# Optimization experiments

Hardware: AMD Instinct MI355X
Metric: run time of the kernel (lower is better)

Reference implementation:

```python
import jax, jax.numpy as jnp
import numpy as np

NL, B, L1, L2, D = 4, 64, 256, 256, 1024
LOGIT_SCALE = 1.0
BN_EPS = 1e-8


def setup_inputs() -> dict:
    key = jax.random.key(0)
    k1, k2, k3, k4, k5, k6 = jax.random.split(key, 6)
    reps1 = jax.random.normal(k1, (NL, B, L1, D), dtype=jnp.float32)
    reps2 = jax.random.normal(k2, (NL, B, L2, D), dtype=jnp.float32)
    len1 = jax.random.randint(k3, (B,), 1, L1 + 1)
    len2 = jax.random.randint(k4, (B,), 1, L2 + 1)
    w = jax.random.normal(k5, (1, NL), dtype=jnp.float32) * 0.1
    b = jax.random.normal(k6, (1,), dtype=jnp.float32) * 0.1
    return {"reps1": reps1, "reps2": reps2, "len1": len1, "len2": len2, "w": w, "b": b}


def reference(reps1, reps2, len1, len2, w, b):
    # reps: (NL, B, L, D) hidden states of selected layers, already (B-major per layer)
    neg = jnp.finfo(reps1.dtype).min
    # cosine-normalize along feature dim
    h1 = reps1 / jnp.linalg.norm(reps1, axis=-1, keepdims=True)
    h2 = reps2 / jnp.linalg.norm(reps2, axis=-1, keepdims=True)
    # similarity matrices for all layers at once: (NL, B, L1, L2)
    dots = jnp.einsum("lbid,lbjd->lbij", h1, h2)
    # ragged validity masks
    mask1 = jnp.arange(L1)[None, :] < len1[:, None]  # (B, L1)
    mask2 = jnp.arange(L2)[None, :] < len2[:, None]  # (B, L2)
    n1 = len1.astype(dots.dtype)
    n2 = len2.astype(dots.dtype)
    # max over valid rows i, mean over valid cols j  -> s1 (NL, B)
    max_i = jnp.max(jnp.where(mask1[None, :, :, None], dots, neg), axis=2)  # (NL,B,L2)
    s1 = jnp.sum(jnp.where(mask2[None], max_i, 0.0), axis=2) / n2[None]
    # max over valid cols j, mean over valid rows i  -> s2 (NL, B)
    max_j = jnp.max(jnp.where(mask2[None, :, None, :], dots, neg), axis=3)  # (NL,B,L1)
    s2 = jnp.sum(jnp.where(mask1[None], max_j, 0.0), axis=2) / n1[None]
    # harmonic mean (F1)
    feat = (2.0 * s1 * s2 / (s1 + s2)).T  # (B, NL)
    # BatchNorm1d(affine=False), training mode: batch stats, biased variance
    mean = jnp.mean(feat, axis=0, keepdims=True)
    var = jnp.mean((feat - mean) ** 2, axis=0, keepdims=True)
    feat = (feat - mean) / jnp.sqrt(var + BN_EPS)
    # final linear head + logit scale -> (B,)
    return LOGIT_SCALE * (feat @ w.T + b)[:, 0]
```

## Files before the change

kernel.cpp:

```cpp
#include <hip/hip_runtime.h>

#define NLAYERS 4
#define BATCH   64
#define LEN1    256
#define LEN2    256
#define DIM     1024
#define BKK     32
#define NKT     (DIM / BKK)
#define PITCH   40

typedef _Float16 f16x8 __attribute__((ext_vector_type(8)));
typedef float    f32x4 __attribute__((ext_vector_type(4)));

__global__ __launch_bounds__(1024, 4)
void bs_main(const float* __restrict__ reps1, const float* __restrict__ reps2,
             const int* __restrict__ len1, const int* __restrict__ len2,
             float* __restrict__ feat) {
  __shared__ _Float16 Ah[2][LEN1 * PITCH];
  __shared__ _Float16 Bh[2][LEN2 * PITCH];
  __shared__ float ssq1[LEN1];
  __shared__ float ssq2[LEN2];
  __shared__ float rowp[LEN1][4];
  __shared__ float colp[LEN2][4];
  __shared__ float redbuf[32];

  const int bid = blockIdx.x;
  const int nl  = bid >> 6;
  const int bb  = bid & 63;
  const float* gA = reps1 + (size_t)bid * LEN1 * DIM;
  const float* gB = reps2 + (size_t)bid * LEN2 * DIM;

  const int tid  = threadIdx.x;
  const int lane = tid & 63;
  const int wid  = tid >> 6;
  const int wm   = wid >> 2;
  const int wn   = wid & 3;
  const int li   = lane & 15;
  const int lh   = lane >> 4;

  if (tid < 256)                  ssq1[tid] = 0.0f;
  else if (tid < 512)             ssq2[tid - 256] = 0.0f;

  f32x4 acc[4][4];
  #pragma unroll
  for (int a = 0; a < 4; ++a)
    #pragma unroll
    for (int c = 0; c < 4; ++c) acc[a][c] = 0.0f;

  float pssqA = 0.f, pssqB = 0.f;
  const int rS = tid >> 2;
  const int cS = (tid & 3) * 8;

  float4 ra[2], rb[2];

  auto issue_loads = [&](int kt) {
    const float4* a4 = (const float4*)(gA + (size_t)rS * DIM + kt * BKK + cS);
    ra[0] = a4[0];  ra[1] = a4[1];
    const float4* b4 = (const float4*)(gB + (size_t)rS * DIM + kt * BKK + cS);
    rb[0] = b4[0];  rb[1] = b4[1];
  };

  auto convert_write = [&](int buf) {
    const int idx = rS * PITCH + cS;
    {
      const float f0 = ra[0].x, f1 = ra[0].y, f2 = ra[0].z, f3 = ra[0].w;
      const float f4 = ra[1].x, f5 = ra[1].y, f6 = ra[1].z, f7 = ra[1].w;
      pssqA += f0*f0 + f1*f1 + f2*f2 + f3*f3 + f4*f4 + f5*f5 + f6*f6 + f7*f7;
      f16x8 hv;
      hv[0] = (_Float16)f0; hv[1] = (_Float16)f1; hv[2] = (_Float16)f2; hv[3] = (_Float16)f3;
      hv[4] = (_Float16)f4; hv[5] = (_Float16)f5; hv[6] = (_Float16)f6; hv[7] = (_Float16)f7;
      *(f16x8*)&Ah[buf][idx] = hv;
    }
    {
      const float f0 = rb[0].x, f1 = rb[0].y, f2 = rb[0].z, f3 = rb[0].w;
      const float f4 = rb[1].x, f5 = rb[1].y, f6 = rb[1].z, f7 = rb[1].w;
      pssqB += f0*f0 + f1*f1 + f2*f2 + f3*f3 + f4*f4 + f5*f5 + f6*f6 + f7*f7;
      f16x8 hv;
      hv[0] = (_Float16)f0; hv[1] = (_Float16)f1; hv[2] = (_Float16)f2; hv[3] = (_Float16)f3;
      hv[4] = (_Float16)f4; hv[5] = (_Float16)f5; hv[6] = (_Float16)f6; hv[7] = (_Float16)f7;
      *(f16x8*)&Bh[buf][idx] = hv;
    }
  };

  issue_loads(0);
  convert_write(0);
  __syncthreads();

  for (int kt = 0; kt < NKT; ++kt) {
    const int cur = kt & 1;
    const bool more = (kt + 1 < NKT);
    if (more) issue_loads(kt + 1);

    const _Float16* AhC = Ah[cur];
    const _Float16* BhC = Bh[cur];
    f16x8 af[4];
    #pragma unroll
    for (int fm = 0; fm < 4; ++fm) {
      const int r = wm * 64 + fm * 16 + li;
      af[fm] = *(const f16x8*)&AhC[r * PITCH + lh * 8];
    }
    #pragma unroll
    for (int fn = 0; fn < 4; ++fn) {
      const int r = wn * 64 + fn * 16 + li;
      const f16x8 bf = *(const f16x8*)&BhC[r * PITCH + lh * 8];
      #pragma unroll
      for (int fm = 0; fm < 4; ++fm)
        acc[fm][fn] = __builtin_amdgcn_mfma_f32_16x16x32_f16(af[fm], bf, acc[fm][fn], 0, 0, 0);
    }

    if (more) convert_write(cur ^ 1);
    __syncthreads();
  }

  atomicAdd(&ssq1[rS], pssqA);
  atomicAdd(&ssq2[rS], pssqB);
  __syncthreads();
  if (tid < 256)       ssq1[tid] = 1.0f / sqrtf(ssq1[tid]);
  else if (tid < 512)  ssq2[tid - 256] = 1.0f / sqrtf(ssq2[tid - 256]);
  __syncthreads();

  const int n1 = len1[bb];
  const int n2 = len2[bb];

  float rn2v[4];
  bool  jv[4];
  #pragma unroll
  for (int fn = 0; fn < 4; ++fn) {
    const int j = wn * 64 + fn * 16 + li;
    rn2v[fn] = ssq2[j];
    jv[fn]   = (j < n2);
  }
  float rn1v[4][4];
  bool  iv[4][4];
  #pragma unroll
  for (int fm = 0; fm < 4; ++fm)
    #pragma unroll
    for (int rg = 0; rg < 4; ++rg) {
      const int i = wm * 64 + fm * 16 + lh * 4 + rg;
      rn1v[fm][rg] = ssq1[i];
      iv[fm][rg]   = (i < n1);
    }

  const float NEG = -3.402823466e38f;
  float rowm[4][4];
  float colm[4];
  #pragma unroll
  for (int fm = 0; fm < 4; ++fm)
    #pragma unroll
    for (int rg = 0; rg < 4; ++rg) rowm[fm][rg] = NEG;
  #pragma unroll
  for (int fn = 0; fn < 4; ++fn) colm[fn] = NEG;

  #pragma unroll
  for (int fm = 0; fm < 4; ++fm)
    #pragma unroll
    for (int fn = 0; fn < 4; ++fn)
      #pragma unroll
      for (int rg = 0; rg < 4; ++rg) {
        const float v = acc[fm][fn][rg] * rn1v[fm][rg] * rn2v[fn];
        if (jv[fn] && v > rowm[fm][rg]) rowm[fm][rg] = v;
        if (iv[fm][rg] && v > colm[fn]) colm[fn] = v;
      }

  #pragma unroll
  for (int m = 1; m <= 8; m <<= 1)
    #pragma unroll
    for (int fm = 0; fm < 4; ++fm)
      #pragma unroll
      for (int rg = 0; rg < 4; ++rg) {
        const float o = __shfl_xor(rowm[fm][rg], m, 64);
        rowm[fm][rg] = fmaxf(rowm[fm][rg], o);
      }
  #pragma unroll
  for (int m = 16; m <= 32; m <<= 1)
    #pragma unroll
    for (int fn = 0; fn < 4; ++fn) {
      const float o = __shfl_xor(colm[fn], m, 64);
      colm[fn] = fmaxf(colm[fn], o);
    }

  if (li == 0)
    #pragma unroll
    for (int fm = 0; fm < 4; ++fm)
      #pragma unroll
      for (int rg = 0; rg < 4; ++rg)
        rowp[wm * 64 + fm * 16 + lh * 4 + rg][wn] = rowm[fm][rg];
  if (lh == 0)
    #pragma unroll
    for (int fn = 0; fn < 4; ++fn)
      colp[wn * 64 + fn * 16 + li][wm] = colm[fn];
  __syncthreads();

  float c1 = 0.f, c2 = 0.f;
  if (tid < 256) {
    const float rm = fmaxf(fmaxf(rowp[tid][0], rowp[tid][1]),
                           fmaxf(rowp[tid][2], rowp[tid][3]));
    if (tid < n1) c2 = rm;
    const float cm = fmaxf(fmaxf(colp[tid][0], colp[tid][1]),
                           fmaxf(colp[tid][2], colp[tid][3]));
    if (tid < n2) c1 = cm;
  }
  #pragma unroll
  for (int m = 1; m <= 32; m <<= 1) {
    c1 += __shfl_xor(c1, m, 64);
    c2 += __shfl_xor(c2, m, 64);
  }
  if (lane == 0) {
    redbuf[wid]      = c1;
    redbuf[16 + wid] = c2;
  }
  __syncthreads();
  if (tid == 0) {
    float s1s = 0.f, s2s = 0.f;
    #pragma unroll
    for (int i = 0; i < 16; ++i) { s1s += redbuf[i]; s2s += redbuf[16 + i]; }
    const float s1 = s1s / (float)n2;
    const float s2 = s2s / (float)n1;
    feat[bb * NLAYERS + nl] = 2.0f * s1 * s2 / (s1 + s2);
  }
}

__global__ void bs_head(const float* __restrict__ feat, const float* __restrict__ w,
                        const float* __restrict__ bias, float* __restrict__ out) {
  __shared__ float lds[NLAYERS][BATCH];
  const int tid = threadIdx.x;
  const int nl  = tid >> 6;
  const int b   = tid & 63;

  const float x = feat[b * NLAYERS + nl];
  float s = x;
  #pragma unroll
  for (int m = 1; m <= 32; m <<= 1) s += __shfl_xor(s, m, 64);
  const float mean = s / 64.0f;
  const float d = x - mean;
  float v = d * d;
  #pragma unroll
  for (int m = 1; m <= 32; m <<= 1) v += __shfl_xor(v, m, 64);
  const float var = v / 64.0f;
  const float y = d / sqrtf(var + 1e-8f);

  lds[nl][b] = y * w[nl];
  __syncthreads();
  if (tid < 64)
    out[tid] = lds[0][tid] + lds[1][tid] + lds[2][tid] + lds[3][tid] + bias[0];
}

extern "C" void kernel_launch(void* const* d_in, const int* in_sizes, int n_in,
                              void* d_out, int out_size, void* d_ws, size_t ws_size,
                              hipStream_t stream) {
  const float* reps1 = (const float*)d_in[0];
  const float* reps2 = (const float*)d_in[1];
  const int*   len1  = (const int*)d_in[2];
  const int*   len2  = (const int*)d_in[3];
  const float* w     = (const float*)d_in[4];
  const float* bias  = (const float*)d_in[5];
  float* feat = (float*)d_ws;

  bs_main<<<NLAYERS * BATCH, 1024, 0, stream>>>(reps1, reps2, len1, len2, feat);
  bs_head<<<1, 256, 0, stream>>>(feat, w, bias, (float*)d_out);
}
```

Measured before the change: 113.1 us.

## Double K-tile depth with XOR-swizzled LDS layout and shuffle-based norm reduction

Raises the K tile from 32 to 64, which halves the number of barrier-separated iterations and doubles the loads in flight per thread. The padded LDS pitch is replaced by an unpadded 64-element pitch with an XOR swizzle on 8-element groups to avoid bank conflicts. The shared-memory atomic accumulation of squared norms becomes a lane shuffle reduction, so the LDS zero-init is no longer needed. LDS use grows (about 128KB for the double-buffered tiles) and register pressure rises with the doubled load buffers, which may hurt occupancy.

```diff
diff --git a/kernel.cpp b/kernel.cpp
--- a/kernel.cpp
+++ b/kernel.cpp
@@ -5,9 +5,9 @@
 #define LEN1    256
 #define LEN2    256
 #define DIM     1024
-#define BKK     32
+#define BKK     64
 #define NKT     (DIM / BKK)
-#define PITCH   40
+#define PITCH   64
 
 typedef _Float16 f16x8 __attribute__((ext_vector_type(8)));
 typedef float    f32x4 __attribute__((ext_vector_type(4)));
@@ -38,9 +38,6 @@
   const int li   = lane & 15;
   const int lh   = lane >> 4;
 
-  if (tid < 256)                  ssq1[tid] = 0.0f;
-  else if (tid < 512)             ssq2[tid - 256] = 0.0f;
-
   f32x4 acc[4][4];
   #pragma unroll
   for (int a = 0; a < 4; ++a)
@@ -49,36 +46,52 @@
 
   float pssqA = 0.f, pssqB = 0.f;
   const int rS = tid >> 2;
-  const int cS = (tid & 3) * 8;
-
-  float4 ra[2], rb[2];
+  const int cq = tid & 3;
+
+  float4 ra[4], rb[4];
 
   auto issue_loads = [&](int kt) {
-    const float4* a4 = (const float4*)(gA + (size_t)rS * DIM + kt * BKK + cS);
-    ra[0] = a4[0];  ra[1] = a4[1];
-    const float4* b4 = (const float4*)(gB + (size_t)rS * DIM + kt * BKK + cS);
-    rb[0] = b4[0];  rb[1] = b4[1];
+    const float4* a4 = (const float4*)(gA + (size_t)rS * DIM + kt * BKK + cq * 16);
+    ra[0] = a4[0];  ra[1] = a4[1];  ra[2] = a4[2];  ra[3] = a4[3];
+    const float4* b4 = (const float4*)(gB + (size_t)rS * DIM + kt * BKK + cq * 16);
+    rb[0] = b4[0];  rb[1] = b4[1];  rb[2] = b4[2];  rb[3] = b4[3];
   };
 
+  const int pc0 = ((2 * cq)     ^ (rS & 7)) * 8;
+  const int pc1 = ((2 * cq + 1) ^ (rS & 7)) * 8;
+
   auto convert_write = [&](int buf) {
-    const int idx = rS * PITCH + cS;
     {
-      const float f0 = ra[0].x, f1 = ra[0].y, f2 = ra[0].z, f3 = ra[0].w;
-      const float f4 = ra[1].x, f5 = ra[1].y, f6 = ra[1].z, f7 = ra[1].w;
-      pssqA += f0*f0 + f1*f1 + f2*f2 + f3*f3 + f4*f4 + f5*f5 + f6*f6 + f7*f7;
-      f16x8 hv;
-      hv[0] = (_Float16)f0; hv[1] = (_Float16)f1; hv[2] = (_Float16)f2; hv[3] = (_Float16)f3;
-      hv[4] = (_Float16)f4; hv[5] = (_Float16)f5; hv[6] = (_Float16)f6; hv[7] = (_Float16)f7;
-      *(f16x8*)&Ah[buf][idx] = hv;
+      f16x8 h0, h1;
+      float s = 0.f;
+      #pragma unroll
+      for (int q = 0; q < 2; ++q) {
+        const float f0 = ra[2*q].x,   f1 = ra[2*q].y,   f2 = ra[2*q].z,   f3 = ra[2*q].w;
+        const float f4 = ra[2*q+1].x, f5 = ra[2*q+1].y, f6 = ra[2*q+1].z, f7 = ra[2*q+1].w;
+        s += f0*f0 + f1*f1 + f2*f2 + f3*f3 + f4*f4 + f5*f5 + f6*f6 + f7*f7;
+        f16x8& hv = q ? h1 : h0;
+        hv[0] = (_Float16)f0; hv[1] = (_Float16)f1; hv[2] = (_Float16)f2; hv[3] = (_Float16)f3;
+        hv[4] = (_Float16)f4; hv[5] = (_Float16)f5; hv[6] = (_Float16)f6; hv[7] = (_Float16)f7;
+      }
+      pssqA += s;
+      *(f16x8*)&Ah[buf][rS * PITCH + pc0] = h0;
+      *(f16x8*)&Ah[buf][rS * PITCH + pc1] = h1;
     }
     {
-      const float f0 = rb[0].x, f1 = rb[0].y, f2 = rb[0].z, f3 = rb[0].w;
-      const float f4 = rb[1].x, f5 = rb[1].y, f6 = rb[1].z, f7 = rb[1].w;
-      pssqB += f0*f0 + f1*f1 + f2*f2 + f3*f3 + f4*f4 + f5*f5 + f6*f6 + f7*f7;
-      f16x8 hv;
-      hv[0] = (_Float16)f0; hv[1] = (_Float16)f1; hv[2] = (_Float16)f2; hv[3] = (_Float16)f3;
-      hv[4] = (_Float16)f4; hv[5] = (_Float16)f5; hv[6] = (_Float16)f6; hv[7] = (_Float16)f7;
-      *(f16x8*)&Bh[buf][idx] = hv;
+      f16x8 h0, h1;
+      float s = 0.f;
+      #pragma unroll
+      for (int q = 0; q < 2; ++q) {
+        const float f0 = rb[2*q].x,   f1 = rb[2*q].y,   f2 = rb[2*q].z,   f3 = rb[2*q].w;
+        const float f4 = rb[2*q+1].x, f5 = rb[2*q+1].y, f6 = rb[2*q+1].z, f7 = rb[2*q+1].w;
+        s += f0*f0 + f1*f1 + f2*f2 + f3*f3 + f4*f4 + f5*f5 + f6*f6 + f7*f7;
+        f16x8& hv = q ? h1 : h0;
+        hv[0] = (_Float16)f0; hv[1] = (_Float16)f1; hv[2] = (_Float16)f2; hv[3] = (_Float16)f3;
+        hv[4] = (_Float16)f4; hv[5] = (_Float16)f5; hv[6] = (_Float16)f6; hv[7] = (_Float16)f7;
+      }
+      pssqB += s;
+      *(f16x8*)&Bh[buf][rS * PITCH + pc0] = h0;
+      *(f16x8*)&Bh[buf][rS * PITCH + pc1] = h1;
     }
   };
 
@@ -93,27 +106,38 @@
 
     const _Float16* AhC = Ah[cur];
     const _Float16* BhC = Bh[cur];
-    f16x8 af[4];
-    #pragma unroll
-    for (int fm = 0; fm < 4; ++fm) {
-      const int r = wm * 64 + fm * 16 + li;
-      af[fm] = *(const f16x8*)&AhC[r * PITCH + lh * 8];
-    }
-    #pragma unroll
-    for (int fn = 0; fn < 4; ++fn) {
-      const int r = wn * 64 + fn * 16 + li;
-      const f16x8 bf = *(const f16x8*)&BhC[r * PITCH + lh * 8];
-      #pragma unroll
-      for (int fm = 0; fm < 4; ++fm)
-        acc[fm][fn] = __builtin_amdgcn_mfma_f32_16x16x32_f16(af[fm], bf, acc[fm][fn], 0, 0, 0);
+    #pragma unroll
+    for (int ks = 0; ks < 2; ++ks) {
+      f16x8 af[4];
+      #pragma unroll
+      for (int fm = 0; fm < 4; ++fm) {
+        const int r = wm * 64 + fm * 16 + li;
+        const int g = ks * 4 + lh;
+        af[fm] = *(const f16x8*)&AhC[r * PITCH + (g ^ (r & 7)) * 8];
+      }
+      #pragma unroll
+      for (int fn = 0; fn < 4; ++fn) {
+        const int r = wn * 64 + fn * 16 + li;
+        const int g = ks * 4 + lh;
+        const f16x8 bf = *(const f16x8*)&BhC[r * PITCH + (g ^ (r & 7)) * 8];
+        #pragma unroll
+        for (int fm = 0; fm < 4; ++fm)
+          acc[fm][fn] = __builtin_amdgcn_mfma_f32_16x16x32_f16(af[fm], bf, acc[fm][fn], 0, 0, 0);
+      }
     }
 
     if (more) convert_write(cur ^ 1);
     __syncthreads();
   }
 
-  atomicAdd(&ssq1[rS], pssqA);
-  atomicAdd(&ssq2[rS], pssqB);
+  pssqA += __shfl_xor(pssqA, 1, 64);
+  pssqA += __shfl_xor(pssqA, 2, 64);
+  pssqB += __shfl_xor(pssqB, 1, 64);
+  pssqB += __shfl_xor(pssqB, 2, 64);
+  if (cq == 0) {
+    ssq1[rS] = pssqA;
+    ssq2[rS] = pssqB;
+  }
   __syncthreads();
   if (tid < 256)       ssq1[tid] = 1.0f / sqrtf(ssq1[tid]);
   else if (tid < 512)  ssq2[tid - 256] = 1.0f / sqrtf(ssq2[tid - 256]);
```

Result: slower. 153.2 us (+35.6%).

## Stage fp32 tiles via direct global-to-LDS DMA with XOR swizzle, convert at fragment load

Applied to the files above, without the earlier changes.

Replaces the register-staged global loads plus fp16 conversion and LDS write with global_load_lds DMA of raw fp32 tiles into a swizzled LDS layout, using manual vmcnt waits and raw barriers. The fp16 conversion moves to MFMA fragment reads, and the sum-of-squares is computed from LDS and reduced with shuffles instead of shared atomics. The aim is to free registers and VALU work from the load path and let the DMA overlap compute. In exchange LDS use doubles (fp32 tiles, 128KB total), each fragment read is converted redundantly across waves, and occupancy may be limited.

```diff
diff --git a/kernel.cpp b/kernel.cpp
--- a/kernel.cpp
+++ b/kernel.cpp
@@ -7,17 +7,31 @@
 #define DIM     1024
 #define BKK     32
 #define NKT     (DIM / BKK)
-#define PITCH   40
 
 typedef _Float16 f16x8 __attribute__((ext_vector_type(8)));
 typedef float    f32x4 __attribute__((ext_vector_type(4)));
+
+typedef __attribute__((address_space(1))) const void gas_void;
+typedef __attribute__((address_space(3))) void       las_void;
+
+__device__ __forceinline__ void dma16(const float* g, float* l) {
+  __builtin_amdgcn_global_load_lds((gas_void*)g, (las_void*)l, 16, 0, 0);
+}
+
+__device__ __forceinline__ void block_bar() {
+  asm volatile("" ::: "memory");
+  __builtin_amdgcn_s_barrier();
+  asm volatile("" ::: "memory");
+}
+
+#define WAITVM(N) asm volatile("s_waitcnt vmcnt(" #N ")" ::: "memory")
 
 __global__ __launch_bounds__(1024, 4)
 void bs_main(const float* __restrict__ reps1, const float* __restrict__ reps2,
              const int* __restrict__ len1, const int* __restrict__ len2,
              float* __restrict__ feat) {
-  __shared__ _Float16 Ah[2][LEN1 * PITCH];
-  __shared__ _Float16 Bh[2][LEN2 * PITCH];
+  __shared__ float Af[2][LEN1 * BKK];
+  __shared__ float Bf[2][LEN2 * BKK];
   __shared__ float ssq1[LEN1];
   __shared__ float ssq2[LEN2];
   __shared__ float rowp[LEN1][4];
@@ -38,82 +52,92 @@
   const int li   = lane & 15;
   const int lh   = lane >> 4;
 
-  if (tid < 256)                  ssq1[tid] = 0.0f;
-  else if (tid < 512)             ssq2[tid - 256] = 0.0f;
-
   f32x4 acc[4][4];
   #pragma unroll
   for (int a = 0; a < 4; ++a)
     #pragma unroll
     for (int c = 0; c < 4; ++c) acc[a][c] = 0.0f;
 
-  float pssqA = 0.f, pssqB = 0.f;
-  const int rS = tid >> 2;
-  const int cS = (tid & 3) * 8;
-
-  float4 ra[2], rb[2];
-
-  auto issue_loads = [&](int kt) {
-    const float4* a4 = (const float4*)(gA + (size_t)rS * DIM + kt * BKK + cS);
-    ra[0] = a4[0];  ra[1] = a4[1];
-    const float4* b4 = (const float4*)(gB + (size_t)rS * DIM + kt * BKK + cS);
-    rb[0] = b4[0];  rb[1] = b4[1];
+  const int r0  = tid >> 3;
+  const int ch0 = tid & 7;
+  const int sc0 = (ch0 ^ (r0 & 7)) << 2;
+  const int sc1 = (ch0 ^ ((r0 + 128) & 7)) << 2;
+
+  float pssqA0 = 0.f, pssqA1 = 0.f, pssqB0 = 0.f, pssqB1 = 0.f;
+
+  auto stage = [&](int kt, int buf) {
+    const int col = kt * BKK;
+    dma16(gA + (size_t)r0 * DIM + col + sc0,          &Af[buf][tid * 4]);
+    dma16(gB + (size_t)r0 * DIM + col + sc0,          &Bf[buf][tid * 4]);
+    dma16(gA + (size_t)(r0 + 128) * DIM + col + sc1,  &Af[buf][(tid + 1024) * 4]);
+    dma16(gB + (size_t)(r0 + 128) * DIM + col + sc1,  &Bf[buf][(tid + 1024) * 4]);
   };
 
-  auto convert_write = [&](int buf) {
-    const int idx = rS * PITCH + cS;
-    {
-      const float f0 = ra[0].x, f1 = ra[0].y, f2 = ra[0].z, f3 = ra[0].w;
-      const float f4 = ra[1].x, f5 = ra[1].y, f6 = ra[1].z, f7 = ra[1].w;
-      pssqA += f0*f0 + f1*f1 + f2*f2 + f3*f3 + f4*f4 + f5*f5 + f6*f6 + f7*f7;
-      f16x8 hv;
-      hv[0] = (_Float16)f0; hv[1] = (_Float16)f1; hv[2] = (_Float16)f2; hv[3] = (_Float16)f3;
-      hv[4] = (_Float16)f4; hv[5] = (_Float16)f5; hv[6] = (_Float16)f6; hv[7] = (_Float16)f7;
-      *(f16x8*)&Ah[buf][idx] = hv;
-    }
-    {
-      const float f0 = rb[0].x, f1 = rb[0].y, f2 = rb[0].z, f3 = rb[0].w;
-      const float f4 = rb[1].x, f5 = rb[1].y, f6 = rb[1].z, f7 = rb[1].w;
-      pssqB += f0*f0 + f1*f1 + f2*f2 + f3*f3 + f4*f4 + f5*f5 + f6*f6 + f7*f7;
-      f16x8 hv;
-      hv[0] = (_Float16)f0; hv[1] = (_Float16)f1; hv[2] = (_Float16)f2; hv[3] = (_Float16)f3;
-      hv[4] = (_Float16)f4; hv[5] = (_Float16)f5; hv[6] = (_Float16)f6; hv[7] = (_Float16)f7;
-      *(f16x8*)&Bh[buf][idx] = hv;
-    }
-  };
-
-  issue_loads(0);
-  convert_write(0);
-  __syncthreads();
-
+  stage(0, 0);
+
+  #pragma unroll 1
   for (int kt = 0; kt < NKT; ++kt) {
     const int cur = kt & 1;
-    const bool more = (kt + 1 < NKT);
-    if (more) issue_loads(kt + 1);
-
-    const _Float16* AhC = Ah[cur];
-    const _Float16* BhC = Bh[cur];
+    if (kt + 1 < NKT) {
+      stage(kt + 1, cur ^ 1);
+      WAITVM(4);
+    } else {
+      WAITVM(0);
+    }
+    block_bar();
+
+    const float* Ac = Af[cur];
+    const float* Bc = Bf[cur];
+
+    {
+      const float4 a0 = *(const float4*)&Ac[tid * 4];
+      const float4 a1 = *(const float4*)&Ac[(tid + 1024) * 4];
+      const float4 b0 = *(const float4*)&Bc[tid * 4];
+      const float4 b1 = *(const float4*)&Bc[(tid + 1024) * 4];
+      pssqA0 += a0.x*a0.x + a0.y*a0.y + a0.z*a0.z + a0.w*a0.w;
+      pssqA1 += a1.x*a1.x + a1.y*a1.y + a1.z*a1.z + a1.w*a1.w;
+      pssqB0 += b0.x*b0.x + b0.y*b0.y + b0.z*b0.z + b0.w*b0.w;
+      pssqB1 += b1.x*b1.x + b1.y*b1.y + b1.z*b1.z + b1.w*b1.w;
+    }
+
     f16x8 af[4];
     #pragma unroll
     for (int fm = 0; fm < 4; ++fm) {
       const int r = wm * 64 + fm * 16 + li;
-      af[fm] = *(const f16x8*)&AhC[r * PITCH + lh * 8];
+      const float4 x0 = *(const float4*)&Ac[r * BKK + ((((lh << 1)    ) ^ (r & 7)) << 2)];
+      const float4 x1 = *(const float4*)&Ac[r * BKK + ((((lh << 1) | 1) ^ (r & 7)) << 2)];
+      f16x8 h;
+      h[0] = (_Float16)x0.x; h[1] = (_Float16)x0.y; h[2] = (_Float16)x0.z; h[3] = (_Float16)x0.w;
+      h[4] = (_Float16)x1.x; h[5] = (_Float16)x1.y; h[6] = (_Float16)x1.z; h[7] = (_Float16)x1.w;
+      af[fm] = h;
     }
     #pragma unroll
     for (int fn = 0; fn < 4; ++fn) {
       const int r = wn * 64 + fn * 16 + li;
-      const f16x8 bf = *(const f16x8*)&BhC[r * PITCH + lh * 8];
+      const float4 y0 = *(const float4*)&Bc[r * BKK + ((((lh << 1)    ) ^ (r & 7)) << 2)];
+      const float4 y1 = *(const float4*)&Bc[r * BKK + ((((lh << 1) | 1) ^ (r & 7)) << 2)];
+      f16x8 bh;
+      bh[0] = (_Float16)y0.x; bh[1] = (_Float16)y0.y; bh[2] = (_Float16)y0.z; bh[3] = (_Float16)y0.w;
+      bh[4] = (_Float16)y1.x; bh[5] = (_Float16)y1.y; bh[6] = (_Float16)y1.z; bh[7] = (_Float16)y1.w;
       #pragma unroll
       for (int fm = 0; fm < 4; ++fm)
-        acc[fm][fn] = __builtin_amdgcn_mfma_f32_16x16x32_f16(af[fm], bf, acc[fm][fn], 0, 0, 0);
-    }
-
-    if (more) convert_write(cur ^ 1);
-    __syncthreads();
-  }
-
-  atomicAdd(&ssq1[rS], pssqA);
-  atomicAdd(&ssq2[rS], pssqB);
+        acc[fm][fn] = __builtin_amdgcn_mfma_f32_16x16x32_f16(af[fm], bh, acc[fm][fn], 0, 0, 0);
+    }
+
+    block_bar();
+  }
+
+  #pragma unroll
+  for (int m = 1; m <= 4; m <<= 1) {
+    pssqA0 += __shfl_xor(pssqA0, m, 64);
+    pssqA1 += __shfl_xor(pssqA1, m, 64);
+    pssqB0 += __shfl_xor(pssqB0, m, 64);
+    pssqB1 += __shfl_xor(pssqB1, m, 64);
+  }
+  if ((lane & 7) == 0) {
+    ssq1[r0] = pssqA0;  ssq1[r0 + 128] = pssqA1;
+    ssq2[r0] = pssqB0;  ssq2[r0 + 128] = pssqB1;
+  }
   __syncthreads();
   if (tid < 256)       ssq1[tid] = 1.0f / sqrtf(ssq1[tid]);
   else if (tid < 512)  ssq2[tid - 256] = 1.0f / sqrtf(ssq2[tid - 256]);
```

After: 127.7 us, median of 2. 12.9% more time.
